# Kernel tuning notes

Measured on AMD Instinct MI355X. Metric: run time of the kernel, lower is better.

## Reference

```python
import jax, jax.numpy as jnp
import numpy as np

jax.config.update("jax_enable_x64", True)

# config
B, S = 4, 4096
H_SIZE = 2048          # hidden_size
VOCAB = 128000         # engram_base_vocab_size
MAX_NGRAM = 3          # engram_max_ngram_size -> orders 2..3
PRIME = 500009         # engram_n_embed_per_ngram (same prime for every order)
N_HEAD = 4             # engram_n_head_per_ngram
E = 32                 # engram_embed_dim
KS = 4                 # short conv kernel size
NUM_ORDERS = MAX_NGRAM - 1
TOTAL_HEADS = NUM_ORDERS * N_HEAD
TOTAL_ROWS = PRIME * N_HEAD * NUM_ORDERS  # flat multi-head table rows


def setup_inputs() -> dict:
    key = jax.random.key(0)
    k_ids, k_h, k_tab, k_cw, k_hp, k_gp, k_op = jax.random.split(key, 7)
    input_ids = jax.random.randint(k_ids, (B, S), 0, VOCAB, dtype=jnp.int64)
    hidden_states = jax.random.normal(k_h, (B, S, H_SIZE), dtype=jnp.float32)
    # identity compressed-tokenizer mapping buffer
    mapping = jnp.arange(VOCAB, dtype=jnp.int64)
    # deterministic odd multipliers, seeded like _build_multipliers
    rng = np.random.default_rng(0 * 10007 + 0 * 1009)
    mults = rng.integers(1, 2 ** 31, size=(NUM_ORDERS, N_HEAD, MAX_NGRAM))
    multipliers = jnp.asarray(mults * 2 + 1, dtype=jnp.int64)
    table = 0.02 * jax.random.normal(k_tab, (TOTAL_ROWS, E), dtype=jnp.float32)
    conv_w = 0.1 * jax.random.normal(k_cw, (E, KS), dtype=jnp.float32)  # depthwise taps
    conv_b = jnp.zeros((E,), dtype=jnp.float32)
    Wh = 0.05 * jax.random.normal(k_hp, (E, TOTAL_HEADS * E), dtype=jnp.float32)
    Wg = 0.02 * jax.random.normal(k_gp, (E, H_SIZE), dtype=jnp.float32)
    Wo = 0.02 * jax.random.normal(k_op, (H_SIZE, E), dtype=jnp.float32)
    return {"input_ids": input_ids, "hidden_states": hidden_states,
            "mapping": mapping, "multipliers": multipliers, "table": table,
            "conv_w": conv_w, "conv_b": conv_b, "Wh": Wh, "Wg": Wg, "Wo": Wo}


def _hash_indices(compressed, multipliers):
    """XOR-mix n-gram hash indices -> [B, S, TOTAL_HEADS] int64."""
    all_idx = []
    offset = 0
    for oi, k in enumerate(range(2, MAX_NGRAM + 1)):
        # forward sliding window, clamped at last token (matches cat/expand trick)
        pos = jnp.minimum(jnp.arange(S)[:, None] + jnp.arange(k)[None, :], S - 1)  # [S,k]
        ng = compressed[:, pos]                                  # [B,S,k]
        m = multipliers[oi, :, :k]                               # [nh,k]
        prod = ng[:, :, None, :] * m[None, None, :, :]           # [B,S,nh,k]
        h = prod[..., 0]
        for p in range(1, k):
            h = h ^ prod[..., p]
        idx = h % PRIME + (offset + jnp.arange(N_HEAD, dtype=jnp.int64) * PRIME)
        all_idx.append(idx)
        offset += PRIME * N_HEAD
    return jnp.concatenate(all_idx, axis=-1)


def reference(input_ids, hidden_states, mapping, multipliers, table,
              conv_w, conv_b, Wh, Wg, Wo):
    compressed = mapping[input_ids]                              # [B,S]
    indices = _hash_indices(compressed, multipliers)             # [B,S,TOTAL_HEADS]
    emb = table[indices].reshape(B, S, TOTAL_HEADS * E)          # multi-head gather
    emb = emb @ Wh.T                                             # head_proj -> [B,S,E]
    # causal depthwise short conv (kernel KS, left pad KS-1)
    xp = jnp.pad(emb, ((0, 0), (KS - 1, 0), (0, 0)))
    emb = sum(xp[:, j:j + S, :] * conv_w[:, j] for j in range(KS)) + conv_b
    gate = jax.nn.sigmoid(hidden_states @ Wg.T)                  # [B,S,E]
    return (gate * emb) @ Wo.T                                   # [B,S,H_SIZE]
```

## Files before the change

### kernel.cpp

```cpp
#include <hip/hip_runtime.h>
#include <stdint.h>

#define HSZ 2048
#define PRIME 500009u

typedef __attribute__((ext_vector_type(8))) short short8;
typedef __attribute__((ext_vector_type(4))) float f32x4;

__device__ __forceinline__ short f2bf(float f) {
  union { float f; unsigned u; } v; v.f = f;
  unsigned u = v.u;
  unsigned r = (u + 0x7FFFu + ((u >> 16) & 1u)) >> 16;
  return (short)(unsigned short)r;
}

__device__ __forceinline__ short8 load8_bf(const float* __restrict__ p) {
  float4 a = *reinterpret_cast<const float4*>(p);
  float4 b = *reinterpret_cast<const float4*>(p + 4);
  short8 r;
  r[0] = f2bf(a.x); r[1] = f2bf(a.y); r[2] = f2bf(a.z); r[3] = f2bf(a.w);
  r[4] = f2bf(b.x); r[5] = f2bf(b.y); r[6] = f2bf(b.z); r[7] = f2bf(b.w);
  return r;
}

__global__ __launch_bounds__(256) void emb0_kernel(
    const int* __restrict__ ids, const int* __restrict__ mapping,
    const unsigned* __restrict__ mult, const float* __restrict__ table,
    const float* __restrict__ Wh, float* __restrict__ emb0) {
  __shared__ __align__(16) short A_lds[32][264];
  __shared__ int idx_lds[256];
  const int tid = threadIdx.x;
  const int t0 = blockIdx.x * 32;

  {
    int t_loc = tid >> 3, head = tid & 7;
    int tg = t0 + t_loc;
    int b = tg >> 12, s = tg & 4095;
    const int* idb = ids + (b << 12);
    int s1 = s + 1 > 4095 ? 4095 : s + 1;
    int s2 = s + 2 > 4095 ? 4095 : s + 2;
    uint64_t c0 = (unsigned)mapping[idb[s]];
    uint64_t c1 = (unsigned)mapping[idb[s1]];
    uint64_t c2 = (unsigned)mapping[idb[s2]];
    int mb = head * 3;
    uint64_t h = (c0 * (uint64_t)mult[mb]) ^ (c1 * (uint64_t)mult[mb + 1]);
    if (head >= 4) h ^= c2 * (uint64_t)mult[mb + 2];
    unsigned row = (unsigned)(h % PRIME) + (unsigned)head * PRIME;
    idx_lds[tid] = (int)row;
  }
  __syncthreads();

  #pragma unroll
  for (int p = 0; p < 8; ++p) {
    int r = p * 32 + (tid >> 3);
    int c4 = (tid & 7) * 4;
    long row = idx_lds[r];
    float4 v = *reinterpret_cast<const float4*>(table + row * 32 + c4);
    int tl = r >> 3, hd = r & 7;
    short* dst = &A_lds[tl][hd * 32 + c4];
    dst[0] = f2bf(v.x); dst[1] = f2bf(v.y); dst[2] = f2bf(v.z); dst[3] = f2bf(v.w);
  }
  __syncthreads();

  int wid = tid >> 6, lane = tid & 63;
  int tt = wid >> 1, e0 = (wid & 1) * 16;
  int l16 = lane & 15, q = lane >> 4;
  short8 Bf[8];
  #pragma unroll
  for (int ks = 0; ks < 8; ++ks)
    Bf[ks] = load8_bf(Wh + (size_t)(e0 + l16) * 256 + ks * 32 + q * 8);
  f32x4 acc = {0.f, 0.f, 0.f, 0.f};
  #pragma unroll
  for (int ks = 0; ks < 8; ++ks) {
    short8 a = *reinterpret_cast<const short8*>(&A_lds[tt * 16 + l16][ks * 32 + q * 8]);
    acc = __builtin_amdgcn_mfma_f32_16x16x32_bf16(a, Bf[ks], acc, 0, 0, 0);
  }
  #pragma unroll
  for (int j = 0; j < 4; ++j) {
    int t = t0 + tt * 16 + q * 4 + j;
    emb0[(size_t)t * 32 + e0 + l16] = acc[j];
  }
}

__global__ __launch_bounds__(256) void fuse_kernel(
    const float* __restrict__ hidden, const float* __restrict__ emb0,
    const float* __restrict__ cw, const float* __restrict__ cb,
    const float* __restrict__ Wg, const float* __restrict__ Wo,
    float* __restrict__ out) {
  __shared__ float emb_lds[32][33];
  __shared__ __align__(16) short ge_lds[32][40];
  __shared__ float accred[2][64][8];
  const int tid = threadIdx.x;
  const int t0 = blockIdx.x * 32;

  #pragma unroll
  for (int it = 0; it < 4; ++it) {
    int ii = it * 256 + tid;
    int tl = ii >> 5, e = ii & 31;
    int s = (t0 + tl) & 4095;
    float a = cb[e];
    #pragma unroll
    for (int j = 0; j < 4; ++j) {
      int sp = s - 3 + j;
      if (sp >= 0) a += cw[e * 4 + j] * emb0[(size_t)(t0 + tl - 3 + j) * 32 + e];
    }
    emb_lds[tl][e] = a;
  }

  int wid = tid >> 6, lane = tid & 63;
  int l16 = lane & 15, q = lane >> 4;
  int tt = wid & 1, kh = wid >> 1;

  f32x4 acc0 = {0, 0, 0, 0}, acc1 = {0, 0, 0, 0};
  const float* hrow = hidden + (size_t)(t0 + tt * 16 + l16) * HSZ + kh * 1024 + q * 8;
  const float* wg0 = Wg + (size_t)l16 * HSZ + kh * 1024 + q * 8;
  const float* wg1 = Wg + (size_t)(16 + l16) * HSZ + kh * 1024 + q * 8;
  for (int kc = 0; kc < 4; ++kc) {
    short8 B0[8], B1[8];
    #pragma unroll
    for (int ks = 0; ks < 8; ++ks) {
      B0[ks] = load8_bf(wg0 + kc * 256 + ks * 32);
      B1[ks] = load8_bf(wg1 + kc * 256 + ks * 32);
    }
    #pragma unroll
    for (int ks = 0; ks < 8; ++ks) {
      short8 a = load8_bf(hrow + kc * 256 + ks * 32);
      acc0 = __builtin_amdgcn_mfma_f32_16x16x32_bf16(a, B0[ks], acc0, 0, 0, 0);
      acc1 = __builtin_amdgcn_mfma_f32_16x16x32_bf16(a, B1[ks], acc1, 0, 0, 0);
    }
  }
  if (kh == 1) {
    #pragma unroll
    for (int j = 0; j < 4; ++j) {
      accred[tt][lane][j] = acc0[j];
      accred[tt][lane][4 + j] = acc1[j];
    }
  }
  __syncthreads();
  if (kh == 0) {
    #pragma unroll
    for (int j = 0; j < 4; ++j) {
      acc0[j] += accred[tt][lane][j];
      acc1[j] += accred[tt][lane][4 + j];
    }
    #pragma unroll
    for (int j = 0; j < 4; ++j) {
      int r = tt * 16 + q * 4 + j;
      float g0 = 1.f / (1.f + __expf(-acc0[j]));
      ge_lds[r][l16] = f2bf(g0 * emb_lds[r][l16]);
      float g1 = 1.f / (1.f + __expf(-acc1[j]));
      ge_lds[r][16 + l16] = f2bf(g1 * emb_lds[r][16 + l16]);
    }
  }
  __syncthreads();

  short8 Af0 = *reinterpret_cast<const short8*>(&ge_lds[l16][q * 8]);
  short8 Af1 = *reinterpret_cast<const short8*>(&ge_lds[16 + l16][q * 8]);
  int hbase = wid * 512;
  for (int ht = 0; ht < 32; ++ht) {
    int h0 = hbase + ht * 16;
    short8 bo = load8_bf(Wo + (size_t)(h0 + l16) * 32 + q * 8);
    f32x4 z = {0, 0, 0, 0};
    f32x4 o0 = __builtin_amdgcn_mfma_f32_16x16x32_bf16(Af0, bo, z, 0, 0, 0);
    f32x4 o1 = __builtin_amdgcn_mfma_f32_16x16x32_bf16(Af1, bo, z, 0, 0, 0);
    #pragma unroll
    for (int j = 0; j < 4; ++j) {
      out[(size_t)(t0 + q * 4 + j) * HSZ + h0 + l16] = o0[j];
      out[(size_t)(t0 + 16 + q * 4 + j) * HSZ + h0 + l16] = o1[j];
    }
  }
}

extern "C" void kernel_launch(void* const* d_in, const int* in_sizes, int n_in,
                              void* d_out, int out_size, void* d_ws, size_t ws_size,
                              hipStream_t stream) {
  const int* ids = (const int*)d_in[0];
  const float* hidden = (const float*)d_in[1];
  const int* mapping = (const int*)d_in[2];
  const unsigned* mult = (const unsigned*)d_in[3];
  const float* table = (const float*)d_in[4];
  const float* cw = (const float*)d_in[5];
  const float* cb = (const float*)d_in[6];
  const float* Wh = (const float*)d_in[7];
  const float* Wg = (const float*)d_in[8];
  const float* Wo = (const float*)d_in[9];
  float* out = (float*)d_out;
  float* emb0 = (float*)d_ws;

  emb0_kernel<<<512, 256, 0, stream>>>(ids, mapping, mult, table, Wh, emb0);
  fuse_kernel<<<512, 256, 0, stream>>>(hidden, emb0, cw, cb, Wg, Wo, out);
}
```

Baseline: 91.58 us.

## Halve tokens per block and split K across all four waves

Both kernels now process 16 tokens per block instead of 32, doubling the grid to 1024 blocks so the 256-CU device gets more waves in flight. The gate GEMM splits the 2048-wide K dimension across all four waves and reduces through LDS, and the head projection splits K in half and reduces the same way. Launch bounds request 4 blocks per CU. The cost is redundant Wg/Wo/Wh weight loads per block, since weights are reused across fewer tokens, plus extra LDS reduction work.

```diff
diff --git a/kernel.cpp b/kernel.cpp
--- a/kernel.cpp
+++ b/kernel.cpp
@@ -23,16 +23,17 @@
   return r;
 }
 
-__global__ __launch_bounds__(256) void emb0_kernel(
+__global__ __launch_bounds__(256, 4) void emb0_kernel(
     const int* __restrict__ ids, const int* __restrict__ mapping,
     const unsigned* __restrict__ mult, const float* __restrict__ table,
     const float* __restrict__ Wh, float* __restrict__ emb0) {
-  __shared__ __align__(16) short A_lds[32][264];
-  __shared__ int idx_lds[256];
+  __shared__ __align__(16) short A_lds[16][264];
+  __shared__ int idx_lds[128];
+  __shared__ float pred[2][64][4];
   const int tid = threadIdx.x;
-  const int t0 = blockIdx.x * 32;
+  const int t0 = blockIdx.x * 16;
 
-  {
+  if (tid < 128) {
     int t_loc = tid >> 3, head = tid & 7;
     int tg = t0 + t_loc;
     int b = tg >> 12, s = tg & 4095;
@@ -51,9 +52,10 @@
   __syncthreads();
 
   #pragma unroll
-  for (int p = 0; p < 8; ++p) {
-    int r = p * 32 + (tid >> 3);
-    int c4 = (tid & 7) * 4;
+  for (int p = 0; p < 4; ++p) {
+    int task = p * 256 + tid;
+    int r = task >> 3;
+    int c4 = (task & 7) * 4;
     long row = idx_lds[r];
     float4 v = *reinterpret_cast<const float4*>(table + row * 32 + c4);
     int tl = r >> 3, hd = r & 7;
@@ -63,38 +65,43 @@
   __syncthreads();
 
   int wid = tid >> 6, lane = tid & 63;
-  int tt = wid >> 1, e0 = (wid & 1) * 16;
+  int e0 = (wid & 1) * 16, kh = wid >> 1;
   int l16 = lane & 15, q = lane >> 4;
-  short8 Bf[8];
-  #pragma unroll
-  for (int ks = 0; ks < 8; ++ks)
-    Bf[ks] = load8_bf(Wh + (size_t)(e0 + l16) * 256 + ks * 32 + q * 8);
   f32x4 acc = {0.f, 0.f, 0.f, 0.f};
   #pragma unroll
-  for (int ks = 0; ks < 8; ++ks) {
-    short8 a = *reinterpret_cast<const short8*>(&A_lds[tt * 16 + l16][ks * 32 + q * 8]);
-    acc = __builtin_amdgcn_mfma_f32_16x16x32_bf16(a, Bf[ks], acc, 0, 0, 0);
+  for (int ks = 0; ks < 4; ++ks) {
+    short8 b = load8_bf(Wh + (size_t)(e0 + l16) * 256 + kh * 128 + ks * 32 + q * 8);
+    short8 a = *reinterpret_cast<const short8*>(&A_lds[l16][kh * 128 + ks * 32 + q * 8]);
+    acc = __builtin_amdgcn_mfma_f32_16x16x32_bf16(a, b, acc, 0, 0, 0);
   }
-  #pragma unroll
-  for (int j = 0; j < 4; ++j) {
-    int t = t0 + tt * 16 + q * 4 + j;
-    emb0[(size_t)t * 32 + e0 + l16] = acc[j];
+  if (kh == 1) {
+    #pragma unroll
+    for (int j = 0; j < 4; ++j) pred[wid & 1][lane][j] = acc[j];
+  }
+  __syncthreads();
+  if (kh == 0) {
+    #pragma unroll
+    for (int j = 0; j < 4; ++j) {
+      float v = acc[j] + pred[wid & 1][lane][j];
+      int t = t0 + q * 4 + j;
+      emb0[(size_t)t * 32 + e0 + l16] = v;
+    }
   }
 }
 
-__global__ __launch_bounds__(256) void fuse_kernel(
+__global__ __launch_bounds__(256, 4) void fuse_kernel(
     const float* __restrict__ hidden, const float* __restrict__ emb0,
     const float* __restrict__ cw, const float* __restrict__ cb,
     const float* __restrict__ Wg, const float* __restrict__ Wo,
     float* __restrict__ out) {
-  __shared__ float emb_lds[32][33];
-  __shared__ __align__(16) short ge_lds[32][40];
-  __shared__ float accred[2][64][8];
+  __shared__ float emb_lds[16][33];
+  __shared__ __align__(16) short ge_lds[16][40];
+  __shared__ float accred[4][8][64];
   const int tid = threadIdx.x;
-  const int t0 = blockIdx.x * 32;
+  const int t0 = blockIdx.x * 16;
 
   #pragma unroll
-  for (int it = 0; it < 4; ++it) {
+  for (int it = 0; it < 2; ++it) {
     int ii = it * 256 + tid;
     int tl = ii >> 5, e = ii & 31;
     int s = (t0 + tl) & 4095;
@@ -109,65 +116,53 @@
 
   int wid = tid >> 6, lane = tid & 63;
   int l16 = lane & 15, q = lane >> 4;
-  int tt = wid & 1, kh = wid >> 1;
 
   f32x4 acc0 = {0, 0, 0, 0}, acc1 = {0, 0, 0, 0};
-  const float* hrow = hidden + (size_t)(t0 + tt * 16 + l16) * HSZ + kh * 1024 + q * 8;
-  const float* wg0 = Wg + (size_t)l16 * HSZ + kh * 1024 + q * 8;
-  const float* wg1 = Wg + (size_t)(16 + l16) * HSZ + kh * 1024 + q * 8;
+  const float* hrow = hidden + (size_t)(t0 + l16) * HSZ + wid * 512 + q * 8;
+  const float* wg0 = Wg + (size_t)l16 * HSZ + wid * 512 + q * 8;
+  const float* wg1 = Wg + (size_t)(16 + l16) * HSZ + wid * 512 + q * 8;
   for (int kc = 0; kc < 4; ++kc) {
-    short8 B0[8], B1[8];
+    short8 B0[4], B1[4], A[4];
     #pragma unroll
-    for (int ks = 0; ks < 8; ++ks) {
-      B0[ks] = load8_bf(wg0 + kc * 256 + ks * 32);
-      B1[ks] = load8_bf(wg1 + kc * 256 + ks * 32);
+    for (int ks = 0; ks < 4; ++ks) {
+      B0[ks] = load8_bf(wg0 + kc * 128 + ks * 32);
+      B1[ks] = load8_bf(wg1 + kc * 128 + ks * 32);
+      A[ks] = load8_bf(hrow + kc * 128 + ks * 32);
     }
     #pragma unroll
-    for (int ks = 0; ks < 8; ++ks) {
-      short8 a = load8_bf(hrow + kc * 256 + ks * 32);
-      acc0 = __builtin_amdgcn_mfma_f32_16x16x32_bf16(a, B0[ks], acc0, 0, 0, 0);
-      acc1 = __builtin_amdgcn_mfma_f32_16x16x32_bf16(a, B1[ks], acc1, 0, 0, 0);
+    for (int ks = 0; ks < 4; ++ks) {
+      acc0 = __builtin_amdgcn_mfma_f32_16x16x32_bf16(A[ks], B0[ks], acc0, 0, 0, 0);
+      acc1 = __builtin_amdgcn_mfma_f32_16x16x32_bf16(A[ks], B1[ks], acc1, 0, 0, 0);
     }
   }
-  if (kh == 1) {
-    #pragma unroll
-    for (int j = 0; j < 4; ++j) {
-      accred[tt][lane][j] = acc0[j];
-      accred[tt][lane][4 + j] = acc1[j];
-    }
-  }
-  __syncthreads();
-  if (kh == 0) {
-    #pragma unroll
-    for (int j = 0; j < 4; ++j) {
-      acc0[j] += accred[tt][lane][j];
-      acc1[j] += accred[tt][lane][4 + j];
-    }
-    #pragma unroll
-    for (int j = 0; j < 4; ++j) {
-      int r = tt * 16 + q * 4 + j;
-      float g0 = 1.f / (1.f + __expf(-acc0[j]));
-      ge_lds[r][l16] = f2bf(g0 * emb_lds[r][l16]);
-      float g1 = 1.f / (1.f + __expf(-acc1[j]));
-      ge_lds[r][16 + l16] = f2bf(g1 * emb_lds[r][16 + l16]);
-    }
+  #pragma unroll
+  for (int j = 0; j < 4; ++j) {
+    accred[wid][j][lane] = acc0[j];
+    accred[wid][4 + j][lane] = acc1[j];
   }
   __syncthreads();
 
-  short8 Af0 = *reinterpret_cast<const short8*>(&ge_lds[l16][q * 8]);
-  short8 Af1 = *reinterpret_cast<const short8*>(&ge_lds[16 + l16][q * 8]);
-  int hbase = wid * 512;
+  #pragma unroll
+  for (int p = 0; p < 2; ++p) {
+    int o = p * 256 + tid;
+    int r = o >> 5, c = o & 31;
+    int ln = (c & 15) + ((r >> 2) << 4);
+    int rg = (r & 3) + ((c >> 4) << 2);
+    float s = accred[0][rg][ln] + accred[1][rg][ln] + accred[2][rg][ln] + accred[3][rg][ln];
+    float g = 1.f / (1.f + __expf(-s));
+    ge_lds[r][c] = f2bf(g * emb_lds[r][c]);
+  }
+  __syncthreads();
+
+  short8 Af = *reinterpret_cast<const short8*>(&ge_lds[l16][q * 8]);
   for (int ht = 0; ht < 32; ++ht) {
-    int h0 = hbase + ht * 16;
+    int h0 = wid * 512 + ht * 16;
     short8 bo = load8_bf(Wo + (size_t)(h0 + l16) * 32 + q * 8);
     f32x4 z = {0, 0, 0, 0};
-    f32x4 o0 = __builtin_amdgcn_mfma_f32_16x16x32_bf16(Af0, bo, z, 0, 0, 0);
-    f32x4 o1 = __builtin_amdgcn_mfma_f32_16x16x32_bf16(Af1, bo, z, 0, 0, 0);
+    f32x4 o0 = __builtin_amdgcn_mfma_f32_16x16x32_bf16(Af, bo, z, 0, 0, 0);
     #pragma unroll
-    for (int j = 0; j < 4; ++j) {
+    for (int j = 0; j < 4; ++j)
       out[(size_t)(t0 + q * 4 + j) * HSZ + h0 + l16] = o0[j];
-      out[(size_t)(t0 + 16 + q * 4 + j) * HSZ + h0 + l16] = o1[j];
-    }
   }
 }
 
@@ -187,6 +182,6 @@
   float* out = (float*)d_out;
   float* emb0 = (float*)d_ws;
 
-  emb0_kernel<<<512, 256, 0, stream>>>(ids, mapping, mult, table, Wh, emb0);
-  fuse_kernel<<<512, 256, 0, stream>>>(hidden, emb0, cw, cb, Wg, Wo, out);
+  emb0_kernel<<<1024, 256, 0, stream>>>(ids, mapping, mult, table, Wh, emb0);
+  fuse_kernel<<<1024, 256, 0, stream>>>(hidden, emb0, cw, cb, Wg, Wo, out);
 }
```

After: 103.7 us. 13.2% more time.
